# Kernel optimization log

Hardware: AMD Instinct MI355X
Metric: run time of the kernel (lower is better)

## Reference

```python
import jax, jax.numpy as jnp
import numpy as np

DIM = 1024
HEADS = 16
HEAD_DIM = DIM // HEADS
HIDDEN = 4 * DIM
SCALE = HEAD_DIM ** -0.5
MASK_VAL = -65504.0
EPS = 1e-5


def layernorm(x, scale, bias):
    mu = jnp.mean(x, axis=-1, keepdims=True)
    var = jnp.mean(jnp.square(x - mu), axis=-1, keepdims=True)
    return (x - mu) * jax.lax.rsqrt(var + EPS) * scale + bias


def setup_inputs() -> dict:
    key = jax.random.key(0)
    ks = jax.random.split(key, 10)
    B, N = 2, 2048
    s = 0.02
    return {
        "x": jax.random.normal(ks[0], (B, N, DIM), jnp.float32),
        "attention_mask": jax.random.randint(ks[1], (B, N), 0, 2) > 0,
        "attention_bias": jax.random.normal(ks[2], (N, N), jnp.float32),
        "qkv_w": jax.random.normal(ks[3], (3 * DIM, DIM), jnp.float32) * s,
        "q_bias": jnp.zeros((DIM,), jnp.float32),
        "v_bias": jnp.zeros((DIM,), jnp.float32),
        "proj_w": jax.random.normal(ks[4], (DIM, DIM), jnp.float32) * s,
        "proj_b": jnp.zeros((DIM,), jnp.float32),
        "ln1_s": jnp.ones((DIM,), jnp.float32),
        "ln1_b": jnp.zeros((DIM,), jnp.float32),
        "ln2_s": jnp.ones((DIM,), jnp.float32),
        "ln2_b": jnp.zeros((DIM,), jnp.float32),
        "fc1_w": jax.random.normal(ks[5], (HIDDEN, DIM), jnp.float32) * s,
        "fc1_b": jnp.zeros((HIDDEN,), jnp.float32),
        "fc2_w": jax.random.normal(ks[6], (DIM, HIDDEN), jnp.float32) * s,
        "fc2_b": jnp.zeros((DIM,), jnp.float32),
    }


def reference(x, attention_mask, attention_bias, qkv_w, q_bias, v_bias,
              proj_w, proj_b, ln1_s, ln1_b, ln2_s, ln2_b,
              fc1_w, fc1_b, fc2_w, fc2_b):
    B, N, C = x.shape
    h = layernorm(x, ln1_s, ln1_b)
    qkv_bias = jnp.concatenate([q_bias, jnp.zeros_like(v_bias), v_bias])
    qkv = h @ qkv_w.T + qkv_bias  # [B,N,3C]
    qkv = qkv.reshape(B, N, 3, HEADS, HEAD_DIM).transpose(2, 0, 3, 1, 4)
    q, k, v = qkv[0], qkv[1], qkv[2]  # [B,H,N,D]
    attn = jnp.einsum('bhnd,bhmd->bhnm', q * SCALE, k)
    mask = attention_mask[:, None, None, :]  # [B,1,1,N]
    attn = jnp.where(mask, MASK_VAL, attn)
    attn = attn + attention_bias[None, None]  # [1,1,N,N] bias
    attn = jax.nn.softmax(attn, axis=-1)
    out = jnp.einsum('bhnm,bhmd->bnhd', attn, v).reshape(B, N, C)
    x_attn = out @ proj_w.T + proj_b
    x = x + x_attn
    h2 = layernorm(x, ln2_s, ln2_b)
    h2 = jax.nn.gelu(h2 @ fc1_w.T + fc1_b, approximate=False)
    x = x + (h2 @ fc2_w.T + fc2_b)
    return (x, attn)
```

## Files before the change

kernel.cpp:

```cpp
#include <hip/hip_runtime.h>
#include <hip/hip_bf16.h>
#include <math.h>

#define NTOK 2048
#define DIM  1024
#define SCALE 0.125f
#define MASK_VAL -65504.0f

typedef __attribute__((ext_vector_type(8))) short bf16x8;
typedef __attribute__((ext_vector_type(4))) float floatx4;

#define MFMA16(a,b,c) __builtin_amdgcn_mfma_f32_16x16x32_bf16((a),(b),(c),0,0,0)
#define GLL16(g,l) __builtin_amdgcn_global_load_lds( \
    (const __attribute__((address_space(1))) void*)(g), \
    (__attribute__((address_space(3))) void*)(l), 16, 0, 0)

__device__ __forceinline__ short f2bf(float f) {
  union { __hip_bfloat16 h; short s; } u;
  u.h = __float2bfloat16(f);
  return u.s;
}
__device__ __forceinline__ float bf2f(short s) {
  union { short s; __hip_bfloat16 h; } u;
  u.s = s;
  return __bfloat162float(u.h);
}

__global__ __launch_bounds__(256) void cvt_bf16(const float* __restrict__ in,
                                                short* __restrict__ out) {
  size_t i = ((size_t)blockIdx.x * 256 + threadIdx.x) * 4;
  float4 v = *(const float4*)(in + i);
  short4 o;
  o.x = f2bf(v.x); o.y = f2bf(v.y); o.z = f2bf(v.z); o.w = f2bf(v.w);
  *(short4*)(out + i) = o;
}

__global__ __launch_bounds__(256) void ln_k(const float* __restrict__ x,
                                            const float* __restrict__ sc,
                                            const float* __restrict__ bi,
                                            short* __restrict__ out) {
  int row = blockIdx.x, t = threadIdx.x;
  float4 v = ((const float4*)(x + (size_t)row * DIM))[t];
  float s  = v.x + v.y + v.z + v.w;
  float s2 = v.x*v.x + v.y*v.y + v.z*v.z + v.w*v.w;
#pragma unroll
  for (int off = 32; off; off >>= 1) {
    s  += __shfl_xor(s, off);
    s2 += __shfl_xor(s2, off);
  }
  __shared__ float ps[4], ps2[4];
  if ((t & 63) == 0) { ps[t >> 6] = s; ps2[t >> 6] = s2; }
  __syncthreads();
  s  = ps[0] + ps[1] + ps[2] + ps[3];
  s2 = ps2[0] + ps2[1] + ps2[2] + ps2[3];
  float mu  = s * (1.0f / DIM);
  float inv = rsqrtf(s2 * (1.0f / DIM) - mu * mu + 1e-5f);
  float4 g = ((const float4*)sc)[t], b = ((const float4*)bi)[t];
  short4 o;
  o.x = f2bf((v.x - mu) * inv * g.x + b.x);
  o.y = f2bf((v.y - mu) * inv * g.y + b.y);
  o.z = f2bf((v.z - mu) * inv * g.z + b.z);
  o.w = f2bf((v.w - mu) * inv * g.w + b.w);
  ((short4*)(out + (size_t)row * DIM))[t] = o;
}

enum { E_QKV = 0, E_RESID = 1, E_FC1 = 2 };

template <int EPI, int K>
__global__ __launch_bounds__(256) void gemm_bt(
    const short* __restrict__ A, const short* __restrict__ B,
    const float* __restrict__ bias0, const float* __restrict__ bias1,
    const float* __restrict__ resid, float* __restrict__ outf,
    short* __restrict__ o0, short* __restrict__ o1, short* __restrict__ o2) {
  __shared__ short As[128 * 32];
  __shared__ short Bs[128 * 32];
  const int t = threadIdx.x;
  const int bm = blockIdx.x, bn = blockIdx.y;
  const int l = t & 63, w = t >> 6;
  const int wr = w >> 1, wc = w & 1;
  const int lr = l & 15, lh = l >> 4;

  const short* ga = A + (size_t)(bm * 128 + (t >> 2)) * K + (t & 3) * 8;
  const short* gb = B + (size_t)(bn * 128 + (t >> 2)) * K + (t & 3) * 8;
  short* la = As + t * 8;
  short* lb = Bs + t * 8;

  floatx4 acc[4][4] = {};
  for (int kb = 0; kb < K / 32; ++kb) {
    GLL16(ga, la);
    GLL16(ga + (size_t)64 * K, la + 2048);
    GLL16(gb, lb);
    GLL16(gb + (size_t)64 * K, lb + 2048);
    ga += 32; gb += 32;
    __syncthreads();
    bf16x8 af[4], bfr[4];
#pragma unroll
    for (int m = 0; m < 4; m++)
      af[m] = *(const bf16x8*)(As + (wr * 64 + m * 16 + lr) * 32 + lh * 8);
#pragma unroll
    for (int n = 0; n < 4; n++)
      bfr[n] = *(const bf16x8*)(Bs + (wc * 64 + n * 16 + lr) * 32 + lh * 8);
#pragma unroll
    for (int m = 0; m < 4; m++)
#pragma unroll
      for (int n = 0; n < 4; n++)
        acc[m][n] = MFMA16(af[m], bfr[n], acc[m][n]);
    __syncthreads();
  }

#pragma unroll
  for (int m = 0; m < 4; m++) {
#pragma unroll
    for (int n = 0; n < 4; n++) {
#pragma unroll
      for (int j = 0; j < 4; j++) {
        int gr = bm * 128 + wr * 64 + m * 16 + lh * 4 + j;
        int gc = bn * 128 + wc * 64 + n * 16 + lr;
        float val = acc[m][n][j];
        if constexpr (EPI == E_QKV) {
          int which = gc >> 10, d = gc & 1023;
          int bb = gr >> 11, n_ = gr & 2047;
          size_t idx = (((size_t)bb * 16 + (d >> 6)) * NTOK + n_) * 64 + (d & 63);
          if (which == 0)      o0[idx] = f2bf((val + bias0[d]) * SCALE);
          else if (which == 1) o1[idx] = f2bf(val);
          else                 o2[idx] = f2bf(val + bias1[d]);
        } else if constexpr (EPI == E_RESID) {
          size_t idx = (size_t)gr * 1024 + gc;
          outf[idx] = val + bias0[gc] + resid[idx];
        } else {
          float u = val + bias0[gc];
          float gelu = 0.5f * u * (1.0f + erff(u * 0.70710678f));
          o0[(size_t)gr * 4096 + gc] = f2bf(gelu);
        }
      }
    }
  }
}

__global__ __launch_bounds__(256) void transpose_v(const short* __restrict__ v,
                                                   short* __restrict__ vt) {
  __shared__ short tile[64][72];
  int bh = blockIdx.x, nb = blockIdx.y, t = threadIdx.x;
  int r = t >> 2, c0 = (t & 3) * 16;
  const short* src = v + ((size_t)bh * NTOK + nb * 64 + r) * 64 + c0;
  *(bf16x8*)&tile[r][c0]     = *(const bf16x8*)src;
  *(bf16x8*)&tile[r][c0 + 8] = *(const bf16x8*)(src + 8);
  __syncthreads();
  int d = t >> 2, n0 = (t & 3) * 16;
  bf16x8 a, b;
#pragma unroll
  for (int i = 0; i < 8; i++) { a[i] = tile[n0 + i][d]; b[i] = tile[n0 + 8 + i][d]; }
  short* dst = vt + ((size_t)bh * 64 + d) * NTOK + nb * 64 + n0;
  *(bf16x8*)dst       = a;
  *(bf16x8*)(dst + 8) = b;
}

__global__ __launch_bounds__(256) void attn_k(
    const short* __restrict__ q, const short* __restrict__ k,
    const short* __restrict__ vt, const int* __restrict__ mask,
    const float* __restrict__ bias, float* __restrict__ attn_out,
    short* __restrict__ out) {
  __shared__ short S[16 * NTOK];
  int blk = blockIdx.x;
  int qt = blk & 127, bh = blk >> 7;
  int b = bh >> 4, h = bh & 15;
  int q0 = qt * 16;
  int t = threadIdx.x, l = t & 63, w = t >> 6;
  int lr = l & 15, lh = l >> 4;

  const short* qb = q + ((size_t)bh * NTOK + q0 + lr) * 64 + lh * 8;
  bf16x8 aq0 = *(const bf16x8*)qb;
  bf16x8 aq1 = *(const bf16x8*)(qb + 32);
  for (int ct = w * 32; ct < w * 32 + 32; ++ct) {
    const short* kb = k + ((size_t)bh * NTOK + ct * 16 + lr) * 64 + lh * 8;
    bf16x8 bk0 = *(const bf16x8*)kb;
    bf16x8 bk1 = *(const bf16x8*)(kb + 32);
    floatx4 s4 = {};
    s4 = MFMA16(aq0, bk0, s4);
    s4 = MFMA16(aq1, bk1, s4);
    int m = ct * 16 + lr;
    int msk = mask[b * NTOK + m];
#pragma unroll
    for (int j = 0; j < 4; j++) {
      int r = lh * 4 + j;
      float val = msk ? MASK_VAL : s4[j];
      val += bias[(size_t)(q0 + r) * NTOK + m];
      *(short*)((char*)S + r * 4096 + ((m * 2) ^ ((r & 7) << 4))) = f2bf(val);
    }
  }
  __syncthreads();

  int r2 = t >> 4, g = t & 15;
  char* Srow = (char*)S + r2 * 4096;
  int swz = (r2 & 7) << 4;
  float mx = -3.0e38f;
#pragma unroll
  for (int i = 0; i < 16; i++) {
    int mb = (g + (i << 4)) << 4;
    bf16x8 p = *(const bf16x8*)(Srow + (mb ^ swz));
#pragma unroll
    for (int j = 0; j < 8; j++) mx = fmaxf(mx, bf2f(p[j]));
  }
#pragma unroll
  for (int off = 8; off; off >>= 1) mx = fmaxf(mx, __shfl_xor(mx, off));
  float sum = 0.f;
#pragma unroll
  for (int i = 0; i < 16; i++) {
    int mb = (g + (i << 4)) << 4;
    bf16x8* pp = (bf16x8*)(Srow + (mb ^ swz));
    bf16x8 p = *pp, e8;
#pragma unroll
    for (int j = 0; j < 8; j++) {
      float e = __expf(bf2f(p[j]) - mx);
      sum += e;
      e8[j] = f2bf(e);
    }
    *pp = e8;
  }
#pragma unroll
  for (int off = 8; off; off >>= 1) sum += __shfl_xor(sum, off);
  float inv = 1.0f / sum;

  float* arow = attn_out + ((size_t)bh * NTOK + q0 + r2) * NTOK;
#pragma unroll
  for (int i = 0; i < 16; i++) {
    int m0 = (g + (i << 4)) << 3;
    bf16x8* pp = (bf16x8*)(Srow + ((m0 * 2) ^ swz));
    bf16x8 p = *pp, pn;
    float4 f0, f1;
    float pv0 = bf2f(p[0]) * inv, pv1 = bf2f(p[1]) * inv,
          pv2 = bf2f(p[2]) * inv, pv3 = bf2f(p[3]) * inv;
    float pv4 = bf2f(p[4]) * inv, pv5 = bf2f(p[5]) * inv,
          pv6 = bf2f(p[6]) * inv, pv7 = bf2f(p[7]) * inv;
    pn[0] = f2bf(pv0); pn[1] = f2bf(pv1); pn[2] = f2bf(pv2); pn[3] = f2bf(pv3);
    pn[4] = f2bf(pv4); pn[5] = f2bf(pv5); pn[6] = f2bf(pv6); pn[7] = f2bf(pv7);
    f0.x = pv0; f0.y = pv1; f0.z = pv2; f0.w = pv3;
    f1.x = pv4; f1.y = pv5; f1.z = pv6; f1.w = pv7;
    *(float4*)(arow + m0)     = f0;
    *(float4*)(arow + m0 + 4) = f1;
    *pp = pn;
  }
  __syncthreads();

  floatx4 o4 = {};
  const short* vtb = vt + ((size_t)bh * 64 + w * 16 + lr) * NTOK;
  char* Sb = (char*)S + lr * 4096;
  int swzr = (lr & 7) << 4;
  for (int kt = 0; kt < 64; ++kt) {
    bf16x8 a  = *(const bf16x8*)(Sb + ((kt * 64 + lh * 16) ^ swzr));
    bf16x8 bv = *(const bf16x8*)(vtb + kt * 32 + lh * 8);
    o4 = MFMA16(a, bv, o4);
  }
#pragma unroll
  for (int j = 0; j < 4; j++) {
    int r = lh * 4 + j;
    out[((size_t)b * NTOK + q0 + r) * DIM + h * 64 + w * 16 + lr] = f2bf(o4[j]);
  }
}

extern "C" void kernel_launch(void* const* d_in, const int* in_sizes, int n_in,
                              void* d_out, int out_size, void* d_ws, size_t ws_size,
                              hipStream_t stream) {
  const float* x      = (const float*)d_in[0];
  const int*   mask   = (const int*)d_in[1];
  const float* abias  = (const float*)d_in[2];
  const float* qkv_w  = (const float*)d_in[3];
  const float* q_bias = (const float*)d_in[4];
  const float* v_bias = (const float*)d_in[5];
  const float* proj_w = (const float*)d_in[6];
  const float* proj_b = (const float*)d_in[7];
  const float* ln1_s  = (const float*)d_in[8];
  const float* ln1_b  = (const float*)d_in[9];
  const float* ln2_s  = (const float*)d_in[10];
  const float* ln2_b  = (const float*)d_in[11];
  const float* fc1_w  = (const float*)d_in[12];
  const float* fc1_b  = (const float*)d_in[13];
  const float* fc2_w  = (const float*)d_in[14];
  const float* fc2_b  = (const float*)d_in[15];

  char* ws = (char*)d_ws;
  short* wq   = (short*)(ws + 0);
  short* wp   = (short*)(ws + 6291456);
  short* w1   = (short*)(ws + 8388608);
  short* w2   = (short*)(ws + 16777216);
  float* x1   = (float*)(ws + 25165824);
  short* hbuf = (short*)(ws + 41943040);
  short* qb   = (short*)(ws + 50331648);
  short* kb   = (short*)(ws + 58720256);
  short* vb   = (short*)(ws + 67108864);
  short* vtb  = (short*)(ws + 75497472);
  short* h3   = (short*)(ws + 50331648);

  float* out_x    = (float*)d_out;
  float* out_attn = (float*)d_out + 4194304;

  cvt_bf16<<<3072, 256, 0, stream>>>(qkv_w, wq);
  cvt_bf16<<<1024, 256, 0, stream>>>(proj_w, wp);
  cvt_bf16<<<4096, 256, 0, stream>>>(fc1_w, w1);
  cvt_bf16<<<4096, 256, 0, stream>>>(fc2_w, w2);

  ln_k<<<4096, 256, 0, stream>>>(x, ln1_s, ln1_b, hbuf);

  gemm_bt<E_QKV, 1024><<<dim3(32, 24), 256, 0, stream>>>(
      hbuf, wq, q_bias, v_bias, nullptr, nullptr, qb, kb, vb);

  transpose_v<<<dim3(32, 32), 256, 0, stream>>>(vb, vtb);

  attn_k<<<4096, 256, 0, stream>>>(qb, kb, vtb, mask, abias, out_attn, hbuf);

  gemm_bt<E_RESID, 1024><<<dim3(32, 8), 256, 0, stream>>>(
      hbuf, wp, proj_b, nullptr, x, x1, nullptr, nullptr, nullptr);

  ln_k<<<4096, 256, 0, stream>>>(x1, ln2_s, ln2_b, hbuf);

  gemm_bt<E_FC1, 1024><<<dim3(32, 32), 256, 0, stream>>>(
      hbuf, w1, fc1_b, nullptr, nullptr, nullptr, h3, nullptr, nullptr);

  gemm_bt<E_RESID, 4096><<<dim3(32, 8), 256, 0, stream>>>(
      h3, w2, fc2_b, nullptr, x1, out_x, nullptr, nullptr, nullptr);
}
```

Before: 1.142 ms.

## Restructure attention kernel with split PV/probability-store warps and narrower output GEMM tiles

The attention kernel moves to 512 threads and computes S^T so the mask and bias can be read as vector int4/float4 loads. It remaps block indices across heads, defers softmax normalization into the PV epilogue, and lets half the warps write the fp32 attention probabilities while the other half run the PV MFMAs. The N=1024 output GEMMs switch to 128x64 tiles so more blocks fill the GPU. The risks are that PV now uses unnormalized bf16 exponentials, which changes rounding slightly, and that the larger block uses more LDS and registers per block.

Result: slower. 1.210 ms (+6.0%).

```diff
diff --git a/kernel.cpp b/kernel.cpp
--- a/kernel.cpp
+++ b/kernel.cpp
@@ -66,42 +66,44 @@
 
 enum { E_QKV = 0, E_RESID = 1, E_FC1 = 2 };
 
-template <int EPI, int K>
+template <int EPI, int K, int BN>
 __global__ __launch_bounds__(256) void gemm_bt(
     const short* __restrict__ A, const short* __restrict__ B,
     const float* __restrict__ bias0, const float* __restrict__ bias1,
     const float* __restrict__ resid, float* __restrict__ outf,
     short* __restrict__ o0, short* __restrict__ o1, short* __restrict__ o2) {
   __shared__ short As[128 * 32];
-  __shared__ short Bs[128 * 32];
+  __shared__ short Bs[BN * 32];
+  constexpr int MI = (BN == 128) ? 4 : 2;
   const int t = threadIdx.x;
   const int bm = blockIdx.x, bn = blockIdx.y;
   const int l = t & 63, w = t >> 6;
-  const int wr = w >> 1, wc = w & 1;
   const int lr = l & 15, lh = l >> 4;
+  const int rowbase = (BN == 128) ? (w >> 1) * 64 : w * 32;
+  const int colbase = (BN == 128) ? (w & 1) * 64 : 0;
 
   const short* ga = A + (size_t)(bm * 128 + (t >> 2)) * K + (t & 3) * 8;
-  const short* gb = B + (size_t)(bn * 128 + (t >> 2)) * K + (t & 3) * 8;
+  const short* gb = B + (size_t)(bn * BN + (t >> 2)) * K + (t & 3) * 8;
   short* la = As + t * 8;
   short* lb = Bs + t * 8;
 
-  floatx4 acc[4][4] = {};
+  floatx4 acc[MI][4] = {};
   for (int kb = 0; kb < K / 32; ++kb) {
     GLL16(ga, la);
     GLL16(ga + (size_t)64 * K, la + 2048);
     GLL16(gb, lb);
-    GLL16(gb + (size_t)64 * K, lb + 2048);
+    if constexpr (BN == 128) GLL16(gb + (size_t)64 * K, lb + 2048);
     ga += 32; gb += 32;
     __syncthreads();
-    bf16x8 af[4], bfr[4];
-#pragma unroll
-    for (int m = 0; m < 4; m++)
-      af[m] = *(const bf16x8*)(As + (wr * 64 + m * 16 + lr) * 32 + lh * 8);
+    bf16x8 af[MI], bfr[4];
+#pragma unroll
+    for (int m = 0; m < MI; m++)
+      af[m] = *(const bf16x8*)(As + (rowbase + m * 16 + lr) * 32 + lh * 8);
 #pragma unroll
     for (int n = 0; n < 4; n++)
-      bfr[n] = *(const bf16x8*)(Bs + (wc * 64 + n * 16 + lr) * 32 + lh * 8);
-#pragma unroll
-    for (int m = 0; m < 4; m++)
+      bfr[n] = *(const bf16x8*)(Bs + (colbase + n * 16 + lr) * 32 + lh * 8);
+#pragma unroll
+    for (int m = 0; m < MI; m++)
 #pragma unroll
       for (int n = 0; n < 4; n++)
         acc[m][n] = MFMA16(af[m], bfr[n], acc[m][n]);
@@ -109,13 +111,13 @@
   }
 
 #pragma unroll
-  for (int m = 0; m < 4; m++) {
+  for (int m = 0; m < MI; m++) {
 #pragma unroll
     for (int n = 0; n < 4; n++) {
 #pragma unroll
       for (int j = 0; j < 4; j++) {
-        int gr = bm * 128 + wr * 64 + m * 16 + lh * 4 + j;
-        int gc = bn * 128 + wc * 64 + n * 16 + lr;
+        int gr = bm * 128 + rowbase + m * 16 + lh * 4 + j;
+        int gc = bn * BN + colbase + n * 16 + lr;
         float val = acc[m][n][j];
         if constexpr (EPI == E_QKV) {
           int which = gc >> 10, d = gc & 1023;
@@ -155,59 +157,64 @@
   *(bf16x8*)(dst + 8) = b;
 }
 
-__global__ __launch_bounds__(256) void attn_k(
+__global__ __launch_bounds__(512) void attn_k(
     const short* __restrict__ q, const short* __restrict__ k,
     const short* __restrict__ vt, const int* __restrict__ mask,
     const float* __restrict__ bias, float* __restrict__ attn_out,
     short* __restrict__ out) {
   __shared__ short S[16 * NTOK];
-  int blk = blockIdx.x;
+  __shared__ float invr[16];
+  int id = blockIdx.x;
+  int blk = (id & 7) * 512 + (id >> 3);
   int qt = blk & 127, bh = blk >> 7;
   int b = bh >> 4, h = bh & 15;
   int q0 = qt * 16;
   int t = threadIdx.x, l = t & 63, w = t >> 6;
   int lr = l & 15, lh = l >> 4;
 
-  const short* qb = q + ((size_t)bh * NTOK + q0 + lr) * 64 + lh * 8;
-  bf16x8 aq0 = *(const bf16x8*)qb;
-  bf16x8 aq1 = *(const bf16x8*)(qb + 32);
-  for (int ct = w * 32; ct < w * 32 + 32; ++ct) {
-    const short* kb = k + ((size_t)bh * NTOK + ct * 16 + lr) * 64 + lh * 8;
-    bf16x8 bk0 = *(const bf16x8*)kb;
-    bf16x8 bk1 = *(const bf16x8*)(kb + 32);
+  const short* qp = q + ((size_t)bh * NTOK + q0 + lr) * 64 + lh * 8;
+  bf16x8 qf0 = *(const bf16x8*)qp;
+  bf16x8 qf1 = *(const bf16x8*)(qp + 32);
+
+  const int* maskb = mask + b * NTOK;
+  for (int i = 0; i < 16; ++i) {
+    int k0 = (w * 16 + i) * 16;
+    const short* kp = k + ((size_t)bh * NTOK + k0 + lr) * 64 + lh * 8;
+    bf16x8 kf0 = *(const bf16x8*)kp;
+    bf16x8 kf1 = *(const bf16x8*)(kp + 32);
     floatx4 s4 = {};
-    s4 = MFMA16(aq0, bk0, s4);
-    s4 = MFMA16(aq1, bk1, s4);
-    int m = ct * 16 + lr;
-    int msk = mask[b * NTOK + m];
-#pragma unroll
-    for (int j = 0; j < 4; j++) {
-      int r = lh * 4 + j;
-      float val = msk ? MASK_VAL : s4[j];
-      val += bias[(size_t)(q0 + r) * NTOK + m];
-      *(short*)((char*)S + r * 4096 + ((m * 2) ^ ((r & 7) << 4))) = f2bf(val);
-    }
+    s4 = MFMA16(kf0, qf0, s4);
+    s4 = MFMA16(kf1, qf1, s4);
+    int m0 = k0 + lh * 4;
+    int4 mk = *(const int4*)(maskb + m0);
+    float4 bv = *(const float4*)(bias + (size_t)(q0 + lr) * NTOK + m0);
+    short4 o;
+    o.x = f2bf((mk.x ? MASK_VAL : s4[0]) + bv.x);
+    o.y = f2bf((mk.y ? MASK_VAL : s4[1]) + bv.y);
+    o.z = f2bf((mk.z ? MASK_VAL : s4[2]) + bv.z);
+    o.w = f2bf((mk.w ? MASK_VAL : s4[3]) + bv.w);
+    *(short4*)((char*)S + lr * 4096 + ((m0 * 2) ^ (lr << 4))) = o;
   }
   __syncthreads();
 
-  int r2 = t >> 4, g = t & 15;
+  int r2 = t >> 5, g = t & 31;
   char* Srow = (char*)S + r2 * 4096;
-  int swz = (r2 & 7) << 4;
+  int swz = r2 << 4;
   float mx = -3.0e38f;
 #pragma unroll
-  for (int i = 0; i < 16; i++) {
-    int mb = (g + (i << 4)) << 4;
-    bf16x8 p = *(const bf16x8*)(Srow + (mb ^ swz));
+  for (int i = 0; i < 8; i++) {
+    int cb = (g + (i << 5)) << 4;
+    bf16x8 p = *(const bf16x8*)(Srow + (cb ^ swz));
 #pragma unroll
     for (int j = 0; j < 8; j++) mx = fmaxf(mx, bf2f(p[j]));
   }
 #pragma unroll
-  for (int off = 8; off; off >>= 1) mx = fmaxf(mx, __shfl_xor(mx, off));
+  for (int off = 16; off; off >>= 1) mx = fmaxf(mx, __shfl_xor(mx, off));
   float sum = 0.f;
 #pragma unroll
-  for (int i = 0; i < 16; i++) {
-    int mb = (g + (i << 4)) << 4;
-    bf16x8* pp = (bf16x8*)(Srow + (mb ^ swz));
+  for (int i = 0; i < 8; i++) {
+    int cb = (g + (i << 5)) << 4;
+    bf16x8* pp = (bf16x8*)(Srow + (cb ^ swz));
     bf16x8 p = *pp, e8;
 #pragma unroll
     for (int j = 0; j < 8; j++) {
@@ -218,43 +225,46 @@
     *pp = e8;
   }
 #pragma unroll
-  for (int off = 8; off; off >>= 1) sum += __shfl_xor(sum, off);
+  for (int off = 16; off; off >>= 1) sum += __shfl_xor(sum, off);
   float inv = 1.0f / sum;
-
-  float* arow = attn_out + ((size_t)bh * NTOK + q0 + r2) * NTOK;
-#pragma unroll
-  for (int i = 0; i < 16; i++) {
-    int m0 = (g + (i << 4)) << 3;
-    bf16x8* pp = (bf16x8*)(Srow + ((m0 * 2) ^ swz));
-    bf16x8 p = *pp, pn;
-    float4 f0, f1;
-    float pv0 = bf2f(p[0]) * inv, pv1 = bf2f(p[1]) * inv,
-          pv2 = bf2f(p[2]) * inv, pv3 = bf2f(p[3]) * inv;
-    float pv4 = bf2f(p[4]) * inv, pv5 = bf2f(p[5]) * inv,
-          pv6 = bf2f(p[6]) * inv, pv7 = bf2f(p[7]) * inv;
-    pn[0] = f2bf(pv0); pn[1] = f2bf(pv1); pn[2] = f2bf(pv2); pn[3] = f2bf(pv3);
-    pn[4] = f2bf(pv4); pn[5] = f2bf(pv5); pn[6] = f2bf(pv6); pn[7] = f2bf(pv7);
-    f0.x = pv0; f0.y = pv1; f0.z = pv2; f0.w = pv3;
-    f1.x = pv4; f1.y = pv5; f1.z = pv6; f1.w = pv7;
-    *(float4*)(arow + m0)     = f0;
-    *(float4*)(arow + m0 + 4) = f1;
-    *pp = pn;
-  }
+  if (g == 0) invr[r2] = inv;
   __syncthreads();
 
-  floatx4 o4 = {};
-  const short* vtb = vt + ((size_t)bh * 64 + w * 16 + lr) * NTOK;
-  char* Sb = (char*)S + lr * 4096;
-  int swzr = (lr & 7) << 4;
-  for (int kt = 0; kt < 64; ++kt) {
-    bf16x8 a  = *(const bf16x8*)(Sb + ((kt * 64 + lh * 16) ^ swzr));
-    bf16x8 bv = *(const bf16x8*)(vtb + kt * 32 + lh * 8);
-    o4 = MFMA16(a, bv, o4);
-  }
-#pragma unroll
-  for (int j = 0; j < 4; j++) {
-    int r = lh * 4 + j;
-    out[((size_t)b * NTOK + q0 + r) * DIM + h * 64 + w * 16 + lr] = f2bf(o4[j]);
+  if (w < 4) {
+    floatx4 o4 = {};
+    const short* vp = vt + ((size_t)bh * 64 + w * 16 + lr) * NTOK + lh * 8;
+    char* Sb = (char*)S + lr * 4096;
+    int pswz = lr << 4;
+    for (int kt = 0; kt < 64; ++kt) {
+      bf16x8 a  = *(const bf16x8*)(Sb + ((kt * 64 + lh * 16) ^ pswz));
+      bf16x8 bv = *(const bf16x8*)(vp + kt * 32);
+      o4 = MFMA16(a, bv, o4);
+    }
+#pragma unroll
+    for (int j = 0; j < 4; ++j) {
+      int r = lh * 4 + j;
+      out[((size_t)b * NTOK + q0 + r) * DIM + h * 64 + w * 16 + lr] =
+          f2bf(o4[j] * invr[r]);
+    }
+  } else {
+    int t2 = t - 256;
+    int rr = t2 >> 4, gg = t2 & 15;
+    char* Sr = (char*)S + rr * 4096;
+    int wswz = rr << 4;
+    float vinv = invr[rr];
+    float* arow = attn_out + ((size_t)bh * NTOK + q0 + rr) * NTOK;
+#pragma unroll
+    for (int i = 0; i < 16; ++i) {
+      int c0 = (gg + (i << 4)) << 3;
+      bf16x8 p = *(const bf16x8*)(Sr + ((c0 * 2) ^ wswz));
+      float4 f0, f1;
+      f0.x = bf2f(p[0]) * vinv; f0.y = bf2f(p[1]) * vinv;
+      f0.z = bf2f(p[2]) * vinv; f0.w = bf2f(p[3]) * vinv;
+      f1.x = bf2f(p[4]) * vinv; f1.y = bf2f(p[5]) * vinv;
+      f1.z = bf2f(p[6]) * vinv; f1.w = bf2f(p[7]) * vinv;
+      *(float4*)(arow + c0)     = f0;
+      *(float4*)(arow + c0 + 4) = f1;
+    }
   }
 }
 
@@ -301,21 +311,21 @@
 
   ln_k<<<4096, 256, 0, stream>>>(x, ln1_s, ln1_b, hbuf);
 
-  gemm_bt<E_QKV, 1024><<<dim3(32, 24), 256, 0, stream>>>(
+  gemm_bt<E_QKV, 1024, 128><<<dim3(32, 24), 256, 0, stream>>>(
       hbuf, wq, q_bias, v_bias, nullptr, nullptr, qb, kb, vb);
 
   transpose_v<<<dim3(32, 32), 256, 0, stream>>>(vb, vtb);
 
-  attn_k<<<4096, 256, 0, stream>>>(qb, kb, vtb, mask, abias, out_attn, hbuf);
-
-  gemm_bt<E_RESID, 1024><<<dim3(32, 8), 256, 0, stream>>>(
+  attn_k<<<4096, 512, 0, stream>>>(qb, kb, vtb, mask, abias, out_attn, hbuf);
+
+  gemm_bt<E_RESID, 1024, 64><<<dim3(32, 16), 256, 0, stream>>>(
       hbuf, wp, proj_b, nullptr, x, x1, nullptr, nullptr, nullptr);
 
   ln_k<<<4096, 256, 0, stream>>>(x1, ln2_s, ln2_b, hbuf);
 
-  gemm_bt<E_FC1, 1024><<<dim3(32, 32), 256, 0, stream>>>(
+  gemm_bt<E_FC1, 1024, 128><<<dim3(32, 32), 256, 0, stream>>>(
       hbuf, w1, fc1_b, nullptr, nullptr, nullptr, h3, nullptr, nullptr);
 
-  gemm_bt<E_RESID, 4096><<<dim3(32, 8), 256, 0, stream>>>(
+  gemm_bt<E_RESID, 4096, 64><<<dim3(32, 16), 256, 0, stream>>>(
       h3, w2, fc2_b, nullptr, x1, out_x, nullptr, nullptr, nullptr);
 }
```
